# Performance work log

Hardware: AMD Instinct MI355X
Metric: run time of the kernel (lower is better)

The kernel has to match this reference:

```python
import jax, jax.numpy as jnp
import numpy as np

B, SEQ, PRED, ENC = 32, 720, 96, 321
LAYERS, SCALE = 2, 2
SEG = [48, 24]
D = [512, 256]
SNX = [SEQ // s for s in SEG]   # [15, 30]
SNY = [PRED // s for s in SEG]  # [2, 4]


def _gru(x, h, Wih, Whh, bih, bhh):
    # torch.nn.GRUCell math
    gi = x @ Wih.T + bih
    gh = h @ Whh.T + bhh
    i_r, i_z, i_n = jnp.split(gi, 3, axis=-1)
    h_r, h_z, h_n = jnp.split(gh, 3, axis=-1)
    r = jax.nn.sigmoid(i_r + h_r)
    z = jax.nn.sigmoid(i_z + h_z)
    n = jnp.tanh(i_n + r * h_n)
    return (1.0 - z) * n + z * h


def setup_inputs():
    key = jax.random.key(0)
    ks = iter(jax.random.split(key, 40))
    inp = {"x": jax.random.normal(next(ks), (B, SEQ, ENC), jnp.float32)}
    sc = 0.02
    for i in range(LAYERS):
        d, s = D[i], SEG[i]
        inp[f"W_emb{i}"] = jax.random.normal(next(ks), (d, s), jnp.float32) * sc
        inp[f"b_emb{i}"] = jnp.zeros((d,), jnp.float32)
        inp[f"Wih{i}"] = jax.random.normal(next(ks), (3 * d, d), jnp.float32) * sc
        inp[f"Whh{i}"] = jax.random.normal(next(ks), (3 * d, d), jnp.float32) * sc
        inp[f"bih{i}"] = jnp.zeros((3 * d,), jnp.float32)
        inp[f"bhh{i}"] = jnp.zeros((3 * d,), jnp.float32)
        inp[f"Wpred{i}"] = jax.random.normal(next(ks), (s, d), jnp.float32) * sc
        inp[f"bpred{i}"] = jnp.zeros((s,), jnp.float32)
        inp[f"pos{i}"] = jax.random.normal(next(ks), (SNY[i], d // 2), jnp.float32)
        inp[f"chan{i}"] = jax.random.normal(next(ks), (ENC, d // 2), jnp.float32)
    return inp


def _forward(x, params):
    seq_last = jax.lax.stop_gradient(x[:, -1:, :])   # [B,1,ENC] (detached in torch)
    xc = (x - seq_last).transpose(0, 2, 1)            # [B,ENC,SEQ]
    out = jnp.zeros((B, PRED, ENC), x.dtype)
    for i in range(LAYERS):
        p = params[i]
        d, s, T, S = D[i], SEG[i], SNX[i], SNY[i]
        # value embedding: [B*ENC, T, seg_len] -> [B*ENC, T, d]
        xe = jax.nn.relu(jnp.einsum('nts,ds->ntd', xc.reshape(-1, T, s), p['W_emb']) + p['b_emb'])
        if i == 0:
            seq = xe.transpose(1, 0, 2)   # all seg_num_x[0] segments in order
        else:
            # faithful to source: finer layer always consumes segments 0..scale^(i+1)-1
            # once per outer step, seg_num_x[0] times in total
            k = SCALE ** (i + 1)
            idx = np.tile(np.arange(k), SNX[0])
            seq = xe[:, idx].transpose(1, 0, 2)
        h0 = jnp.zeros((xe.shape[0], d), x.dtype)
        step = lambda h, xt: (_gru(xt, h, p['Wih'], p['Whh'], p['bih'], p['bhh']), None)
        h_fin, _ = jax.lax.scan(step, h0, seq)   # [B*ENC, d]
        # decoder: seg_num_y independent GRU cell applications (no carried state)
        half = d // 2
        pos = jnp.concatenate([
            jnp.broadcast_to(p['pos'][None], (ENC, S, half)),
            jnp.broadcast_to(p['chan'][:, None], (ENC, S, half))], axis=-1).reshape(ENC * S, d)
        pos = jnp.tile(pos, (B, 1)).reshape(S, B * ENC, d)   # contiguous chunks per step
        hn = jnp.repeat(h_fin, S, axis=0).reshape(S, B * ENC, d)
        hy = _gru(pos, hn, p['Wih'], p['Whh'], p['bih'], p['bhh'])   # [S, B*ENC, d]
        y = hy.reshape(S * B * ENC, d) @ p['Wpred'].T + p['bpred']   # [S*B*ENC, seg_len]
        y = y.reshape(-1, ENC, PRED).transpose(0, 2, 1)              # [B, PRED, ENC]
        out = out + y + seq_last
    return out / LAYERS


def reference(x, W_emb0, b_emb0, Wih0, Whh0, bih0, bhh0, Wpred0, bpred0, pos0, chan0,
              W_emb1, b_emb1, Wih1, Whh1, bih1, bhh1, Wpred1, bpred1, pos1, chan1):
    params = [
        dict(W_emb=W_emb0, b_emb=b_emb0, Wih=Wih0, Whh=Whh0, bih=bih0, bhh=bhh0,
             Wpred=Wpred0, bpred=bpred0, pos=pos0, chan=chan0),
        dict(W_emb=W_emb1, b_emb=b_emb1, Wih=Wih1, Whh=Whh1, bih=bih1, bhh=bhh1,
             Wpred=Wpred1, bpred=bpred1, pos=pos1, chan=chan1),
    ]
    return _forward(x, params)
```

## Files before the change

### kernel.cpp

```cpp
#include <hip/hip_runtime.h>
#include <math.h>


#define NB     10272
#define MP     10368
#define ENC_   321
#define SEQ_   720
#define PRED_  96
#define BATCH_ 32

typedef long long i64;
typedef unsigned short u16;
typedef unsigned int u32;
using bf16x8 = __attribute__((ext_vector_type(8))) short;
using f32x4  = __attribute__((ext_vector_type(4))) float;

#define AS1 __attribute__((address_space(1)))
#define AS3 __attribute__((address_space(3)))
#define GLOAD16(g, l) __builtin_amdgcn_global_load_lds((const AS1 void*)(g), (AS3 void*)(l), 16, 0, 0)

__device__ __forceinline__ float bf2f(u16 u) {
    union { u32 i; float f; } v; v.i = ((u32)u) << 16; return v.f;
}
__device__ __forceinline__ u16 f2bf(float f) {
    union { float f; u32 i; } v; v.f = f;
    return (u16)((v.i + 0x7fff + ((v.i >> 16) & 1)) >> 16);
}
__device__ __forceinline__ float sigf(float x) {
    x = fminf(fmaxf(x, -30.f), 30.f);
    return 1.f / (1.f + __expf(-x));
}
__device__ __forceinline__ float tanhfast(float x) {
    x = fminf(fmaxf(x, -15.f), 15.f);
    float e = __expf(2.f * x);
    return (e - 1.f) / (e + 1.f);
}
__device__ __forceinline__ void swz(int idx, int NXT, int NYT, int& mt, int& nt) {
    int per = NYT * 8;
    int grp = idx / per;
    int base = grp * 8;
    int mg = NXT - base; if (mg > 8) mg = 8;
    int rem = idx - grp * per;
    mt = base + rem % mg;
    nt = rem / mg;
}

__global__ __launch_bounds__(256) void zero2_kernel(float* __restrict__ a,
                                                    u16* __restrict__ b, i64 n) {
    i64 i = (i64)blockIdx.x * 256 + threadIdx.x;
    if (i < n) { a[i] = 0.f; b[i] = 0; }
}

__global__ __launch_bounds__(256) void convert_pad(const float* __restrict__ src,
                                                   u16* __restrict__ dst,
                                                   int R, int C, int Rp, int Cp) {
    i64 idx = (i64)blockIdx.x * 256 + threadIdx.x;
    i64 total = (i64)Rp * Cp;
    if (idx >= total) return;
    int r = (int)(idx / Cp);
    int c = (int)(idx - (i64)r * Cp);
    dst[idx] = (r < R && c < C) ? f2bf(src[(i64)r * C + c]) : (u16)0;
}

__global__ __launch_bounds__(256) void seg_gather_bf(const float* __restrict__ x,
                                                     u16* __restrict__ dst,
                                                     int t0, int T, int s, int Kp) {
    i64 idx = (i64)blockIdx.x * 256 + threadIdx.x;
    i64 per_t = (i64)MP * Kp;
    i64 total = (i64)T * per_t;
    if (idx >= total) return;
    int t = (int)(idx / per_t);
    i64 rem = idx - (i64)t * per_t;
    int j = (int)(rem / MP);
    int n = (int)(rem - (i64)j * MP);
    float v = 0.f;
    if (n < NB && j < s) {
        int b = n / ENC_, e = n - b * ENC_;
        const float* xb = x + (i64)b * SEQ_ * ENC_ + e;
        v = xb[(i64)((t0 + t) * s + j) * ENC_] - xb[(i64)(SEQ_ - 1) * ENC_];
    }
    dst[((i64)t * MP + n) * Kp + j] = f2bf(v);
}

__global__ __launch_bounds__(256) void pmat_fill_bf(const float* __restrict__ pos,
                                                    const float* __restrict__ chan,
                                                    u16* __restrict__ dst,
                                                    int S, int d, int Rp) {
    i64 idx = (i64)blockIdx.x * 256 + threadIdx.x;
    i64 total = (i64)Rp * d;
    if (idx >= total) return;
    int row = (int)(idx / d);
    int c = (int)(idx - (i64)row * d);
    float v = 0.f;
    if (row < ENC_ * S) {
        int e = row / S, sy = row - e * S;
        int half = d >> 1;
        v = (c < half) ? pos[sy * half + c] : chan[e * half + (c - half)];
    }
    dst[idx] = f2bf(v);
}

__global__ __launch_bounds__(256) void out_kernel(const float* __restrict__ x,
                                                  const float* __restrict__ y0,
                                                  const float* __restrict__ y1,
                                                  float* __restrict__ out) {
    int idx = blockIdx.x * 256 + threadIdx.x;
    const int total = BATCH_ * PRED_ * ENC_;
    if (idx >= total) return;
    int b = idx / (PRED_ * ENC_);
    int r = idx - b * (PRED_ * ENC_);
    int p = r / ENC_;
    int e = r - p * ENC_;
    int n = b * ENC_ + e;
    float sl = x[(i64)b * SEQ_ * ENC_ + (i64)(SEQ_ - 1) * ENC_ + e];
    out[idx] = sl + 0.5f * (y0[(i64)n * PRED_ + p] + y1[(i64)n * PRED_ + p]);
}

template<int MODE>
__global__ __launch_bounds__(256) void gemm_bf16mfma(const u16* __restrict__ A,
                                                     const u16* __restrict__ B,
                                                     const float* __restrict__ bias,
                                                     void* __restrict__ Cp,
                                                     int K, int Mstore, int Nstore,
                                                     int ldc, int NXT, int NYT) {
    __shared__ u16 smA[128 * 64];
    __shared__ u16 smB[128 * 64];
    const int tid = threadIdx.x;
    const int w = tid >> 6, l = tid & 63;
    int mt, nt; swz(blockIdx.x, NXT, NYT, mt, nt);
    const int m0 = mt * 128, n0 = nt * 128;
    const int srow = (l >> 3) & 7, pch = l & 7;
    const int cch = pch ^ srow;
    const u16* ga[4]; const u16* gb[4];
#pragma unroll
    for (int r = 0; r < 4; ++r) {
        int seg = r * 4 + w;
        ga[r] = A + (i64)(m0 + seg * 8 + srow) * K + cch * 8;
        gb[r] = B + (i64)(n0 + seg * 8 + srow) * K + cch * 8;
    }
    f32x4 acc[4][4] = {};
    const int lr = l & 15, lg = l >> 4;
    const int wm = (w >> 1) * 64, wn = (w & 1) * 64;
    for (int kk = 0; kk < K; kk += 64) {
#pragma unroll
        for (int r = 0; r < 4; ++r) { GLOAD16(ga[r], smA + (r * 4 + w) * 512); ga[r] += 64; }
#pragma unroll
        for (int r = 0; r < 4; ++r) { GLOAD16(gb[r], smB + (r * 4 + w) * 512); gb[r] += 64; }
        __syncthreads();
#pragma unroll
        for (int s = 0; s < 2; ++s) {
            const int ph = ((s * 4 + lg) ^ (lr & 7)) * 8;
            bf16x8 av[4], bv[4];
#pragma unroll
            for (int i = 0; i < 4; ++i)
                av[i] = *(const bf16x8*)(smA + (wm + i * 16 + lr) * 64 + ph);
#pragma unroll
            for (int j = 0; j < 4; ++j)
                bv[j] = *(const bf16x8*)(smB + (wn + j * 16 + lr) * 64 + ph);
#pragma unroll
            for (int i = 0; i < 4; ++i)
#pragma unroll
                for (int j = 0; j < 4; ++j)
                    acc[i][j] = __builtin_amdgcn_mfma_f32_16x16x32_bf16(av[i], bv[j], acc[i][j], 0, 0, 0);
        }
        __syncthreads();
    }
#pragma unroll
    for (int i = 0; i < 4; ++i) {
        int mbase = m0 + wm + i * 16 + 4 * lg;
#pragma unroll
        for (int j = 0; j < 4; ++j) {
            int c = n0 + wn + j * 16 + lr;
            if (c >= Nstore) continue;
            float bs = bias[c];
#pragma unroll
            for (int r = 0; r < 4; ++r) {
                int mm = mbase + r;
                if (mm < Mstore) {
                    float v = acc[i][j][r] + bs;
                    if (MODE == 2) v = fmaxf(v, 0.f);
                    if (MODE == 0) ((float*)Cp)[(i64)mm * ldc + c] = v;
                    else           ((u16*)Cp)[(i64)mm * ldc + c] = f2bf(v);
                }
            }
        }
    }
}

template<int D>
__global__ __launch_bounds__(256, 3) void gru_step(const u16* __restrict__ xe,
                                                   const u16* __restrict__ hsrc,
                                                   const u16* __restrict__ Wih,
                                                   const u16* __restrict__ Whh,
                                                   const float* __restrict__ bih,
                                                   const float* __restrict__ bhh,
                                                   f32x4* __restrict__ hfrag,
                                                   u16* __restrict__ hdst) {
    constexpr int NCT = D / 16;
    __shared__ u16 smA[64 * 64];
    __shared__ u16 smB[3 * 64 * 64];
    const int tid = threadIdx.x;
    const int w = tid >> 6, l = tid & 63;
    const int m0 = blockIdx.x * 64;
    const int c0 = blockIdx.y * 64;
    const int srow = (l >> 3) & 7, pch = l & 7;
    const int cch = pch ^ srow;
    const int lr = l & 15, lg = l >> 4;
    f32x4 aR[4] = {}, aZ[4] = {}, aNI[4] = {}, aNH[4] = {};
#pragma unroll
    for (int phase = 0; phase < 2; ++phase) {
        const u16* Abase = phase ? hsrc : xe;
        const u16* Bbase = phase ? Whh : Wih;
        const u16* ga[2]; const u16* gb[6];
#pragma unroll
        for (int r = 0; r < 2; ++r)
            ga[r] = Abase + (i64)(m0 + (r * 4 + w) * 8 + srow) * D + cch * 8;
#pragma unroll
        for (int q = 0; q < 6; ++q) {
            int gs = q * 4 + w;
            int g = gs >> 3, sp = gs & 7;
            gb[q] = Bbase + (i64)(g * D + c0 + sp * 8 + srow) * D + cch * 8;
        }
        for (int kk = 0; kk < D; kk += 64) {
#pragma unroll
            for (int r = 0; r < 2; ++r) { GLOAD16(ga[r], smA + (r * 4 + w) * 512); ga[r] += 64; }
#pragma unroll
            for (int q = 0; q < 6; ++q) { GLOAD16(gb[q], smB + (q * 4 + w) * 512); gb[q] += 64; }
            __syncthreads();
#pragma unroll
            for (int s = 0; s < 2; ++s) {
                const int phs = ((s * 4 + lg) ^ (lr & 7)) * 8;
                bf16x8 av = *(const bf16x8*)(smA + (w * 16 + lr) * 64 + phs);
#pragma unroll
                for (int j = 0; j < 4; ++j) {
                    bf16x8 b0 = *(const bf16x8*)(smB + 0 * 4096 + (j * 16 + lr) * 64 + phs);
                    bf16x8 b1 = *(const bf16x8*)(smB + 1 * 4096 + (j * 16 + lr) * 64 + phs);
                    bf16x8 b2 = *(const bf16x8*)(smB + 2 * 4096 + (j * 16 + lr) * 64 + phs);
                    aR[j] = __builtin_amdgcn_mfma_f32_16x16x32_bf16(av, b0, aR[j], 0, 0, 0);
                    aZ[j] = __builtin_amdgcn_mfma_f32_16x16x32_bf16(av, b1, aZ[j], 0, 0, 0);
                    if (phase == 0)
                        aNI[j] = __builtin_amdgcn_mfma_f32_16x16x32_bf16(av, b2, aNI[j], 0, 0, 0);
                    else
                        aNH[j] = __builtin_amdgcn_mfma_f32_16x16x32_bf16(av, b2, aNH[j], 0, 0, 0);
                }
            }
            __syncthreads();
        }
    }
    const int Trow = (m0 >> 4) + w;
    const int rowb = m0 + w * 16 + 4 * lg;
#pragma unroll
    for (int j = 0; j < 4; ++j) {
        const int cc = c0 + j * 16 + lr;
        const i64 tb = (i64)Trow * NCT + ((c0 >> 4) + j);
        f32x4 ho = hfrag[tb * 64 + l];
        float bR = bih[cc] + bhh[cc];
        float bZ = bih[D + cc] + bhh[D + cc];
        float bNI = bih[2 * D + cc];
        float bNH = bhh[2 * D + cc];
        f32x4 hn;
#pragma unroll
        for (int r = 0; r < 4; ++r) {
            float rr = sigf(aR[j][r] + bR);
            float zz = sigf(aZ[j][r] + bZ);
            float nn = tanhfast(aNI[j][r] + bNI + rr * (aNH[j][r] + bNH));
            hn[r] = (1.f - zz) * nn + zz * ho[r];
        }
        hfrag[tb * 64 + l] = hn;
#pragma unroll
        for (int r = 0; r < 4; ++r)
            hdst[(i64)(rowb + r) * D + cc] = f2bf(hn[r]);
    }
}

template<int D>
__global__ __launch_bounds__(256, 3) void gru_step_h(const u16* __restrict__ gi,
                                                     const u16* __restrict__ hsrc,
                                                     const u16* __restrict__ Whh,
                                                     const float* __restrict__ bhh,
                                                     f32x4* __restrict__ hfrag,
                                                     u16* __restrict__ hdst) {
    constexpr int NCT = D / 16;
    __shared__ u16 smA[64 * 64];
    __shared__ u16 smB[3 * 64 * 64];
    const int tid = threadIdx.x;
    const int w = tid >> 6, l = tid & 63;
    const int m0 = blockIdx.x * 64;
    const int c0 = blockIdx.y * 64;
    const int srow = (l >> 3) & 7, pch = l & 7;
    const int cch = pch ^ srow;
    const int lr = l & 15, lg = l >> 4;
    f32x4 aR[4] = {}, aZ[4] = {}, aNH[4] = {};
    const u16* ga[2]; const u16* gb[6];
#pragma unroll
    for (int r = 0; r < 2; ++r)
        ga[r] = hsrc + (i64)(m0 + (r * 4 + w) * 8 + srow) * D + cch * 8;
#pragma unroll
    for (int q = 0; q < 6; ++q) {
        int gs = q * 4 + w;
        int g = gs >> 3, sp = gs & 7;
        gb[q] = Whh + (i64)(g * D + c0 + sp * 8 + srow) * D + cch * 8;
    }
    for (int kk = 0; kk < D; kk += 64) {
#pragma unroll
        for (int r = 0; r < 2; ++r) { GLOAD16(ga[r], smA + (r * 4 + w) * 512); ga[r] += 64; }
#pragma unroll
        for (int q = 0; q < 6; ++q) { GLOAD16(gb[q], smB + (q * 4 + w) * 512); gb[q] += 64; }
        __syncthreads();
#pragma unroll
        for (int s = 0; s < 2; ++s) {
            const int phs = ((s * 4 + lg) ^ (lr & 7)) * 8;
            bf16x8 av = *(const bf16x8*)(smA + (w * 16 + lr) * 64 + phs);
#pragma unroll
            for (int j = 0; j < 4; ++j) {
                bf16x8 b0 = *(const bf16x8*)(smB + 0 * 4096 + (j * 16 + lr) * 64 + phs);
                bf16x8 b1 = *(const bf16x8*)(smB + 1 * 4096 + (j * 16 + lr) * 64 + phs);
                bf16x8 b2 = *(const bf16x8*)(smB + 2 * 4096 + (j * 16 + lr) * 64 + phs);
                aR[j] = __builtin_amdgcn_mfma_f32_16x16x32_bf16(av, b0, aR[j], 0, 0, 0);
                aZ[j] = __builtin_amdgcn_mfma_f32_16x16x32_bf16(av, b1, aZ[j], 0, 0, 0);
                aNH[j] = __builtin_amdgcn_mfma_f32_16x16x32_bf16(av, b2, aNH[j], 0, 0, 0);
            }
        }
        __syncthreads();
    }
    const int Trow = (m0 >> 4) + w;
    const int rowb = m0 + w * 16 + 4 * lg;
#pragma unroll
    for (int j = 0; j < 4; ++j) {
        const int cc = c0 + j * 16 + lr;
        const i64 tb = (i64)Trow * NCT + ((c0 >> 4) + j);
        f32x4 ho = hfrag[tb * 64 + l];
        float bR = bhh[cc];
        float bZ = bhh[D + cc];
        float bNH = bhh[2 * D + cc];
        f32x4 hn;
#pragma unroll
        for (int r = 0; r < 4; ++r) {
            const u16* gp = gi + (i64)(rowb + r) * 3 * D + cc;
            float rr = sigf(bf2f(gp[0]) + aR[j][r] + bR);
            float zz = sigf(bf2f(gp[D]) + aZ[j][r] + bZ);
            float nn = tanhfast(bf2f(gp[2 * D]) + rr * (aNH[j][r] + bNH));
            hn[r] = (1.f - zz) * nn + zz * ho[r];
        }
        hfrag[tb * 64 + l] = hn;
#pragma unroll
        for (int r = 0; r < 4; ++r)
            hdst[(i64)(rowb + r) * D + cc] = f2bf(hn[r]);
    }
}

template<int D, int S>
__global__ __launch_bounds__(256) void gru_dec(const u16* __restrict__ Asrc,
                                               const u16* __restrict__ Whh,
                                               const float* __restrict__ bhh,
                                               const u16* __restrict__ gi,
                                               const f32x4* __restrict__ hfrag,
                                               u16* __restrict__ hy) {
    constexpr int NCT = D / 16;
    constexpr int NYT = D / 64;
    __shared__ u16 smA[128 * 64];
    __shared__ u16 smB[3 * 64 * 64];
    const int tid = threadIdx.x;
    const int w = tid >> 6, l = tid & 63;
    int mt, nt; swz(blockIdx.x, 81, NYT, mt, nt);
    const int m0 = mt * 128;
    const int c0 = nt * 64;
    const int srow = (l >> 3) & 7, pch = l & 7;
    const int cch = pch ^ srow;
    const u16* ga[4]; const u16* gb[6];
#pragma unroll
    for (int r = 0; r < 4; ++r)
        ga[r] = Asrc + (i64)(m0 + (r * 4 + w) * 8 + srow) * D + cch * 8;
#pragma unroll
    for (int q = 0; q < 6; ++q) {
        int gs = q * 4 + w;
        int g = gs >> 3, sp = gs & 7;
        gb[q] = Whh + (i64)(g * D + c0 + sp * 8 + srow) * D + cch * 8;
    }
    f32x4 acc[3][4][2] = {};
    const int lr = l & 15, lg = l >> 4;
    const int wm = (w >> 1) * 64, wc = (w & 1) * 32;
    for (int kk = 0; kk < D; kk += 64) {
#pragma unroll
        for (int r = 0; r < 4; ++r) { GLOAD16(ga[r], smA + (r * 4 + w) * 512); ga[r] += 64; }
#pragma unroll
        for (int q = 0; q < 6; ++q) { GLOAD16(gb[q], smB + (q * 4 + w) * 512); gb[q] += 64; }
        __syncthreads();
#pragma unroll
        for (int s = 0; s < 2; ++s) {
            const int ph = ((s * 4 + lg) ^ (lr & 7)) * 8;
            bf16x8 av[4], bv[3][2];
#pragma unroll
            for (int i = 0; i < 4; ++i)
                av[i] = *(const bf16x8*)(smA + (wm + i * 16 + lr) * 64 + ph);
#pragma unroll
            for (int g = 0; g < 3; ++g)
#pragma unroll
                for (int j = 0; j < 2; ++j)
                    bv[g][j] = *(const bf16x8*)(smB + g * 4096 + (wc + j * 16 + lr) * 64 + ph);
#pragma unroll
            for (int g = 0; g < 3; ++g)
#pragma unroll
                for (int i = 0; i < 4; ++i)
#pragma unroll
                    for (int j = 0; j < 2; ++j)
                        acc[g][i][j] = __builtin_amdgcn_mfma_f32_16x16x32_bf16(av[i], bv[g][j], acc[g][i][j], 0, 0, 0);
        }
        __syncthreads();
    }
#pragma unroll
    for (int i = 0; i < 4; ++i) {
        const int Trow = (m0 + wm + 16 * i) >> 4;
        const int rowb = m0 + wm + 16 * i + 4 * lg;
#pragma unroll
        for (int j = 0; j < 2; ++j) {
            const int cc = c0 + wc + 16 * j + lr;
            const int ct = (c0 + wc + 16 * j) >> 4;
            const i64 tb = (i64)Trow * NCT + ct;
            float b0 = bhh[cc], b1 = bhh[D + cc], b2 = bhh[2 * D + cc];
            f32x4 ho = hfrag[tb * 64 + l];
#pragma unroll
            for (int r = 0; r < 4; ++r) {
                int mm = rowb + r;
                if (mm >= NB) continue;
                int e = mm % ENC_;
                float hr = acc[0][i][j][r] + b0;
                float hz = acc[1][i][j][r] + b1;
                float hn2 = acc[2][i][j][r] + b2;
#pragma unroll
                for (int sy = 0; sy < S; ++sy) {
                    i64 gib = (i64)(e * S + sy) * 3 * D + cc;
                    float rr = sigf(bf2f(gi[gib]) + hr);
                    float zz = sigf(bf2f(gi[gib + D]) + hz);
                    float nn = tanhfast(bf2f(gi[gib + 2 * D]) + rr * hn2);
                    hy[((i64)mm * S + sy) * D + cc] = f2bf((1.f - zz) * nn + zz * ho[r]);
                }
            }
        }
    }
}

extern "C" void kernel_launch(void* const* d_in, const int* in_sizes, int n_in,
                              void* d_out, int out_size, void* d_ws, size_t ws_size,
                              hipStream_t stream) {
    const float* x      = (const float*)d_in[0];
    const float* W_emb0 = (const float*)d_in[1];
    const float* b_emb0 = (const float*)d_in[2];
    const float* Wih0   = (const float*)d_in[3];
    const float* Whh0   = (const float*)d_in[4];
    const float* bih0   = (const float*)d_in[5];
    const float* bhh0   = (const float*)d_in[6];
    const float* Wpred0 = (const float*)d_in[7];
    const float* bpred0 = (const float*)d_in[8];
    const float* pos0   = (const float*)d_in[9];
    const float* chan0  = (const float*)d_in[10];
    const float* W_emb1 = (const float*)d_in[11];
    const float* b_emb1 = (const float*)d_in[12];
    const float* Wih1   = (const float*)d_in[13];
    const float* Whh1   = (const float*)d_in[14];
    const float* bih1   = (const float*)d_in[15];
    const float* bhh1   = (const float*)d_in[16];
    const float* Wpred1 = (const float*)d_in[17];
    const float* bpred1 = (const float*)d_in[18];
    const float* pos1   = (const float*)d_in[19];
    const float* chan1  = (const float*)d_in[20];
    float* out = (float*)d_out;

    i64 off = 0;
    char* base = (char*)d_ws;
    auto alloc = [&](i64 bytes) -> void* {
        void* p = base + off; off += (bytes + 255) & ~(i64)255; return p;
    };
    float* f_hfrag = (float*)alloc((i64)MP * 512 * 4);
    u16*   f_mirA  = (u16*)  alloc((i64)MP * 512 * 2);
    u16*   f_mirB  = (u16*)  alloc((i64)MP * 512 * 2);
    u16*   wih0b   = (u16*)  alloc((i64)1536 * 512 * 2);
    u16*   whh0b   = (u16*)  alloc((i64)1536 * 512 * 2);
    u16*   wih1b   = (u16*)  alloc((i64)768 * 256 * 2);
    u16*   whh1b   = (u16*)  alloc((i64)768 * 256 * 2);
    u16*   we0b    = (u16*)  alloc((i64)512 * 64 * 2);
    u16*   we1b    = (u16*)  alloc((i64)256 * 64 * 2);
    u16*   wp0b    = (u16*)  alloc((i64)128 * 512 * 2);
    u16*   wp1b    = (u16*)  alloc((i64)128 * 256 * 2);
    u16*   f_pm0   = (u16*)  alloc((i64)768 * 512 * 2);
    u16*   f_pm1   = (u16*)  alloc((i64)1408 * 256 * 2);
    u16*   f_gidec = (u16*)  alloc((i64)768 * 1536 * 2);
    u16*   f_hy    = (u16*)  alloc((i64)4 * NB * 256 * 2);
    float* f_y0    = (float*)alloc((i64)NB * 96 * 4);
    float* f_y1    = (float*)alloc((i64)NB * 96 * 4);
    i64 fixed = off;

    char* R = base + fixed;
    i64 a1 = (((i64)4 * MP * 64 * 2) + 255) & ~(i64)255;
    i64 a2 = (((i64)4 * MP * 256 * 2) + 255) & ~(i64)255;
    i64 a3 = (i64)4 * MP * 768 * 2;
    i64 R1 = a1 + a2 + a3;
    u16* f_seg1 = (u16*)R;
    u16* f_xe1  = (u16*)(R + a1);
    u16* f_gi1  = (u16*)(R + a1 + a2);
    int gsz = 1;
    {
        const int cand[4] = {15, 5, 3, 2};
        for (int ii = 0; ii < 4; ++ii) {
            i64 need = (i64)cand[ii] * MP * (64 + 512) * 2 + 2 * 256;
            i64 tot = fixed + (need > R1 ? need : R1);
            if (tot <= (i64)ws_size) { gsz = cand[ii]; break; }
        }
    }
    u16* f_seg0 = (u16*)R;
    i64 s1 = (((i64)gsz * MP * 64 * 2) + 255) & ~(i64)255;
    u16* f_xe0 = (u16*)(R + s1);

    auto cvt = [&](const float* s, u16* dst, int Rr, int C, int Rp, int Cp) {
        i64 tot = (i64)Rp * Cp;
        convert_pad<<<(int)((tot + 255) / 256), 256, 0, stream>>>(s, dst, Rr, C, Rp, Cp);
    };
    auto gemmN = [&](const u16* A, const u16* B, const float* bias, void* C,
                     int gx, int Nc, int K, int Mstore, int ldc, int mode) {
        int NYT = (Nc + 127) / 128;
        dim3 g(gx * NYT);
        if (mode == 0)      gemm_bf16mfma<0><<<g, 256, 0, stream>>>(A, B, bias, C, K, Mstore, Nc, ldc, gx, NYT);
        else if (mode == 1) gemm_bf16mfma<1><<<g, 256, 0, stream>>>(A, B, bias, C, K, Mstore, Nc, ldc, gx, NYT);
        else                gemm_bf16mfma<2><<<g, 256, 0, stream>>>(A, B, bias, C, K, Mstore, Nc, ldc, gx, NYT);
    };

    cvt(Wih0, wih0b, 1536, 512, 1536, 512);
    cvt(Whh0, whh0b, 1536, 512, 1536, 512);
    cvt(Wih1, wih1b, 768, 256, 768, 256);
    cvt(Whh1, whh1b, 768, 256, 768, 256);
    cvt(W_emb0, we0b, 512, 48, 512, 64);
    cvt(W_emb1, we1b, 256, 24, 256, 64);
    cvt(Wpred0, wp0b, 48, 512, 128, 512);
    cvt(Wpred1, wp1b, 24, 256, 128, 256);
    pmat_fill_bf<<<(int)(((i64)768 * 512 + 255) / 256), 256, 0, stream>>>(pos0, chan0, f_pm0, 2, 512, 768);
    pmat_fill_bf<<<(int)(((i64)1408 * 256 + 255) / 256), 256, 0, stream>>>(pos1, chan1, f_pm1, 4, 256, 1408);

    {
        i64 n = (i64)MP * 512;
        zero2_kernel<<<(int)((n + 255) / 256), 256, 0, stream>>>(f_hfrag, f_mirA, n);
    }
    for (int t0 = 0; t0 < 15;) {
        int g = 15 - t0 < gsz ? 15 - t0 : gsz;
        i64 tot = (i64)g * MP * 64;
        seg_gather_bf<<<(int)((tot + 255) / 256), 256, 0, stream>>>(x, f_seg0, t0, g, 48, 64);
        gemmN(f_seg0, we0b, b_emb0, f_xe0, g * 81, 512, 64, g * MP, 512, 2);
        for (int s = 0; s < g; ++s) {
            int tg = t0 + s;
            const u16* Asrc = (tg & 1) ? f_mirB : f_mirA;
            u16* Adst = (tg & 1) ? f_mirA : f_mirB;
            gru_step<512><<<dim3(162, 8), 256, 0, stream>>>(
                f_xe0 + (i64)s * MP * 512, Asrc, wih0b, whh0b, bih0, bhh0,
                (f32x4*)f_hfrag, Adst);
        }
        t0 += g;
    }
    gemmN(f_pm0, wih0b, bih0, f_gidec, 6, 1536, 512, 642, 1536, 1);
    gru_dec<512, 2><<<dim3(81 * 8), 256, 0, stream>>>(
        f_mirB, whh0b, bhh0, f_gidec, (const f32x4*)f_hfrag, f_hy);
    gemmN(f_hy, wp0b, bpred0, f_y0, 161, 48, 512, 2 * NB, 48, 0);

    {
        i64 n = (i64)MP * 256;
        zero2_kernel<<<(int)((n + 255) / 256), 256, 0, stream>>>(f_hfrag, f_mirA, n);
    }
    {
        i64 tot = (i64)4 * MP * 64;
        seg_gather_bf<<<(int)((tot + 255) / 256), 256, 0, stream>>>(x, f_seg1, 0, 4, 24, 64);
    }
    gemmN(f_seg1, we1b, b_emb1, f_xe1, 324, 256, 64, 4 * MP, 256, 2);
    gemmN(f_xe1, wih1b, bih1, f_gi1, 324, 768, 256, 4 * MP, 768, 1);
    for (int t = 0; t < 60; ++t) {
        const u16* Asrc = (t & 1) ? f_mirB : f_mirA;
        u16* Adst = (t & 1) ? f_mirA : f_mirB;
        gru_step_h<256><<<dim3(162, 4), 256, 0, stream>>>(
            f_gi1 + (i64)(t & 3) * MP * 768, Asrc, whh1b, bhh1,
            (f32x4*)f_hfrag, Adst);
    }
    gemmN(f_pm1, wih1b, bih1, f_gidec, 11, 768, 256, 1284, 768, 1);
    gru_dec<256, 4><<<dim3(81 * 4), 256, 0, stream>>>(
        f_mirA, whh1b, bhh1, f_gidec, (const f32x4*)f_hfrag, f_hy);
    gemmN(f_hy, wp1b, bpred1, f_y1, 321, 24, 256, 4 * NB, 24, 0);

    out_kernel<<<(BATCH_ * PRED_ * ENC_ + 255) / 256, 256, 0, stream>>>(x, f_y0, f_y1, out);
}
```

Baseline: 2.373 ms.

## Fuse layer-1 GRU recurrence into a persistent scan kernel with LDS-resident state

Replaces 60 per-step gru_step_h launches with one gru_scan kernel. Each block owns 64 rows across all 256 columns, keeps the hidden state in registers and a double-buffered LDS copy, and streams Whh tiles through a triple-buffered global_load_lds pipeline. This removes per-step launch overhead, the global round-trip of the hidden state, and the separate zeroing kernel. The cost is only 162 blocks (less parallelism than 162x4), and Whh is re-streamed by every block at every step.

New measurement: 3.997 ms. 1.68x slower.

```diff
diff --git a/kernel.cpp b/kernel.cpp
--- a/kernel.cpp
+++ b/kernel.cpp
@@ -18,6 +18,7 @@
 #define AS1 __attribute__((address_space(1)))
 #define AS3 __attribute__((address_space(3)))
 #define GLOAD16(g, l) __builtin_amdgcn_global_load_lds((const AS1 void*)(g), (AS3 void*)(l), 16, 0, 0)
+#define MFMA16(a, b, c) __builtin_amdgcn_mfma_f32_16x16x32_bf16(a, b, c, 0, 0, 0)
 
 __device__ __forceinline__ float bf2f(u16 u) {
     union { u32 i; float f; } v; v.i = ((u32)u) << 16; return v.f;
@@ -161,7 +162,7 @@
             for (int i = 0; i < 4; ++i)
 #pragma unroll
                 for (int j = 0; j < 4; ++j)
-                    acc[i][j] = __builtin_amdgcn_mfma_f32_16x16x32_bf16(av[i], bv[j], acc[i][j], 0, 0, 0);
+                    acc[i][j] = MFMA16(av[i], bv[j], acc[i][j]);
         }
         __syncthreads();
     }
@@ -236,12 +237,12 @@
                     bf16x8 b0 = *(const bf16x8*)(smB + 0 * 4096 + (j * 16 + lr) * 64 + phs);
                     bf16x8 b1 = *(const bf16x8*)(smB + 1 * 4096 + (j * 16 + lr) * 64 + phs);
                     bf16x8 b2 = *(const bf16x8*)(smB + 2 * 4096 + (j * 16 + lr) * 64 + phs);
-                    aR[j] = __builtin_amdgcn_mfma_f32_16x16x32_bf16(av, b0, aR[j], 0, 0, 0);
-                    aZ[j] = __builtin_amdgcn_mfma_f32_16x16x32_bf16(av, b1, aZ[j], 0, 0, 0);
+                    aR[j] = MFMA16(av, b0, aR[j]);
+                    aZ[j] = MFMA16(av, b1, aZ[j]);
                     if (phase == 0)
-                        aNI[j] = __builtin_amdgcn_mfma_f32_16x16x32_bf16(av, b2, aNI[j], 0, 0, 0);
+                        aNI[j] = MFMA16(av, b2, aNI[j]);
                     else
-                        aNH[j] = __builtin_amdgcn_mfma_f32_16x16x32_bf16(av, b2, aNH[j], 0, 0, 0);
+                        aNH[j] = MFMA16(av, b2, aNH[j]);
                 }
             }
             __syncthreads();
@@ -273,79 +274,116 @@
     }
 }
 
-template<int D>
-__global__ __launch_bounds__(256, 3) void gru_step_h(const u16* __restrict__ gi,
-                                                     const u16* __restrict__ hsrc,
-                                                     const u16* __restrict__ Whh,
-                                                     const float* __restrict__ bhh,
-                                                     f32x4* __restrict__ hfrag,
-                                                     u16* __restrict__ hdst) {
+template<int D, int T>
+__global__ __launch_bounds__(256) void gru_scan(const u16* __restrict__ gi,
+                                                const u16* __restrict__ Whh,
+                                                const float* __restrict__ bhh,
+                                                f32x4* __restrict__ hfrag,
+                                                u16* __restrict__ hdst) {
     constexpr int NCT = D / 16;
-    __shared__ u16 smA[64 * 64];
-    __shared__ u16 smB[3 * 64 * 64];
+    __shared__ u16 hb[2][4][64 * 64];
+    __shared__ u16 sB[3][192 * 64];
     const int tid = threadIdx.x;
     const int w = tid >> 6, l = tid & 63;
     const int m0 = blockIdx.x * 64;
-    const int c0 = blockIdx.y * 64;
     const int srow = (l >> 3) & 7, pch = l & 7;
     const int cch = pch ^ srow;
     const int lr = l & 15, lg = l >> 4;
-    f32x4 aR[4] = {}, aZ[4] = {}, aNH[4] = {};
-    const u16* ga[2]; const u16* gb[6];
-#pragma unroll
-    for (int r = 0; r < 2; ++r)
-        ga[r] = hsrc + (i64)(m0 + (r * 4 + w) * 8 + srow) * D + cch * 8;
+    const int rowl = w * 16 + 4 * lg;
+
+    const u16* gq[6];
 #pragma unroll
     for (int q = 0; q < 6; ++q) {
         int gs = q * 4 + w;
-        int g = gs >> 3, sp = gs & 7;
-        gb[q] = Whh + (i64)(g * D + c0 + sp * 8 + srow) * D + cch * 8;
-    }
-    for (int kk = 0; kk < D; kk += 64) {
-#pragma unroll
-        for (int r = 0; r < 2; ++r) { GLOAD16(ga[r], smA + (r * 4 + w) * 512); ga[r] += 64; }
-#pragma unroll
-        for (int q = 0; q < 6; ++q) { GLOAD16(gb[q], smB + (q * 4 + w) * 512); gb[q] += 64; }
-        __syncthreads();
-#pragma unroll
-        for (int s = 0; s < 2; ++s) {
-            const int phs = ((s * 4 + lg) ^ (lr & 7)) * 8;
-            bf16x8 av = *(const bf16x8*)(smA + (w * 16 + lr) * 64 + phs);
+        int gate = gs >> 3, sp = gs & 7;
+        gq[q] = Whh + (i64)(gate * D + sp * 8 + srow) * D + cch * 8;
+    }
+    f32x4 hm[4][4];
+#pragma unroll
+    for (int a = 0; a < 4; ++a)
+#pragma unroll
+        for (int b = 0; b < 4; ++b) hm[a][b] = f32x4{0.f, 0.f, 0.f, 0.f};
+    {
+        u32* p = (u32*)&hb[0][0][0];
+        for (int i = tid; i < 8192; i += 256) p[i] = 0;
+    }
+    auto STAGE = [&](int g) {
+        int s16 = g & 15;
+        i64 off = (i64)((s16 >> 2) * 64) * D + (i64)(s16 & 3) * 64;
+        u16* dst = &sB[g % 3][0];
+#pragma unroll
+        for (int q = 0; q < 6; ++q)
+            GLOAD16(gq[q] + off, dst + (q * 4 + w) * 512);
+    };
+    STAGE(0); STAGE(1);
+
+    for (int t = 0; t < T; ++t) {
+        const int hcur = t & 1, hnxt = hcur ^ 1;
+        const u16* gis = gi + (i64)(t & 3) * MP * 3 * D;
+#pragma unroll
+        for (int c0i = 0; c0i < 4; ++c0i) {
+            f32x4 aR[4] = {}, aZ[4] = {}, aNH[4] = {};
+#pragma unroll
+            for (int kk = 0; kk < 4; ++kk) {
+                asm volatile("s_waitcnt vmcnt(6) lgkmcnt(0)" ::: "memory");
+                __builtin_amdgcn_s_barrier();
+                __builtin_amdgcn_sched_barrier(0);
+                const int g = t * 16 + c0i * 4 + kk;
+                STAGE(g + 2);
+                const u16* bp = &sB[g % 3][0];
+                const u16* ap = &hb[hcur][kk][0];
+#pragma unroll
+                for (int s = 0; s < 2; ++s) {
+                    const int phs = ((s * 4 + lg) ^ (lr & 7)) * 8;
+                    bf16x8 av = *(const bf16x8*)(ap + (w * 16 + lr) * 64 + phs);
+#pragma unroll
+                    for (int j = 0; j < 4; ++j) {
+                        bf16x8 b0 = *(const bf16x8*)(bp + (0 * 64 + j * 16 + lr) * 64 + phs);
+                        bf16x8 b1 = *(const bf16x8*)(bp + (1 * 64 + j * 16 + lr) * 64 + phs);
+                        bf16x8 b2 = *(const bf16x8*)(bp + (2 * 64 + j * 16 + lr) * 64 + phs);
+                        aR[j] = MFMA16(av, b0, aR[j]);
+                        aZ[j] = MFMA16(av, b1, aZ[j]);
+                        aNH[j] = MFMA16(av, b2, aNH[j]);
+                    }
+                }
+            }
 #pragma unroll
             for (int j = 0; j < 4; ++j) {
-                bf16x8 b0 = *(const bf16x8*)(smB + 0 * 4096 + (j * 16 + lr) * 64 + phs);
-                bf16x8 b1 = *(const bf16x8*)(smB + 1 * 4096 + (j * 16 + lr) * 64 + phs);
-                bf16x8 b2 = *(const bf16x8*)(smB + 2 * 4096 + (j * 16 + lr) * 64 + phs);
-                aR[j] = __builtin_amdgcn_mfma_f32_16x16x32_bf16(av, b0, aR[j], 0, 0, 0);
-                aZ[j] = __builtin_amdgcn_mfma_f32_16x16x32_bf16(av, b1, aZ[j], 0, 0, 0);
-                aNH[j] = __builtin_amdgcn_mfma_f32_16x16x32_bf16(av, b2, aNH[j], 0, 0, 0);
+                const int cc = c0i * 64 + j * 16 + lr;
+                const float bR = bhh[cc];
+                const float bZ = bhh[D + cc];
+                const float bN = bhh[2 * D + cc];
+#pragma unroll
+                for (int r = 0; r < 4; ++r) {
+                    const u16* gp = gis + (i64)(m0 + rowl + r) * 3 * D + cc;
+                    float rr = sigf(bf2f(gp[0]) + aR[j][r] + bR);
+                    float zz = sigf(bf2f(gp[D]) + aZ[j][r] + bZ);
+                    float nn = tanhfast(bf2f(gp[2 * D]) + rr * (aNH[j][r] + bN));
+                    hm[c0i][j][r] = (1.f - zz) * nn + zz * hm[c0i][j][r];
+                }
+                const int cl = j * 16 + lr;
+#pragma unroll
+                for (int r = 0; r < 4; ++r) {
+                    const int row = rowl + r;
+                    hb[hnxt][c0i][row * 64 + (((cl >> 3) ^ (row & 7)) << 3) + (cl & 7)]
+                        = f2bf(hm[c0i][j][r]);
+                }
             }
         }
-        __syncthreads();
-    }
-    const int Trow = (m0 >> 4) + w;
-    const int rowb = m0 + w * 16 + 4 * lg;
-#pragma unroll
-    for (int j = 0; j < 4; ++j) {
-        const int cc = c0 + j * 16 + lr;
-        const i64 tb = (i64)Trow * NCT + ((c0 >> 4) + j);
-        f32x4 ho = hfrag[tb * 64 + l];
-        float bR = bhh[cc];
-        float bZ = bhh[D + cc];
-        float bNH = bhh[2 * D + cc];
-        f32x4 hn;
-#pragma unroll
-        for (int r = 0; r < 4; ++r) {
-            const u16* gp = gi + (i64)(rowb + r) * 3 * D + cc;
-            float rr = sigf(bf2f(gp[0]) + aR[j][r] + bR);
-            float zz = sigf(bf2f(gp[D]) + aZ[j][r] + bZ);
-            float nn = tanhfast(bf2f(gp[2 * D]) + rr * (aNH[j][r] + bNH));
-            hn[r] = (1.f - zz) * nn + zz * ho[r];
-        }
-        hfrag[tb * 64 + l] = hn;
-#pragma unroll
-        for (int r = 0; r < 4; ++r)
-            hdst[(i64)(rowb + r) * D + cc] = f2bf(hn[r]);
+        if (t == T - 1) {
+            const int Trow = (m0 >> 4) + w;
+#pragma unroll
+            for (int c0i = 0; c0i < 4; ++c0i)
+#pragma unroll
+                for (int j = 0; j < 4; ++j) {
+                    const i64 tb = (i64)Trow * NCT + (c0i * 4 + j);
+                    hfrag[tb * 64 + l] = hm[c0i][j];
+                    const int cc = c0i * 64 + j * 16 + lr;
+#pragma unroll
+                    for (int r = 0; r < 4; ++r)
+                        hdst[(i64)(m0 + rowl + r) * D + cc] = f2bf(hm[c0i][j][r]);
+                }
+        }
     }
 }
 
@@ -404,7 +442,7 @@
                 for (int i = 0; i < 4; ++i)
 #pragma unroll
                     for (int j = 0; j < 2; ++j)
-                        acc[g][i][j] = __builtin_amdgcn_mfma_f32_16x16x32_bf16(av[i], bv[g][j], acc[g][i][j], 0, 0, 0);
+                        acc[g][i][j] = MFMA16(av[i], bv[g][j], acc[g][i][j]);
         }
         __syncthreads();
     }
@@ -560,22 +598,13 @@
     gemmN(f_hy, wp0b, bpred0, f_y0, 161, 48, 512, 2 * NB, 48, 0);
 
     {
-        i64 n = (i64)MP * 256;
-        zero2_kernel<<<(int)((n + 255) / 256), 256, 0, stream>>>(f_hfrag, f_mirA, n);
-    }
-    {
         i64 tot = (i64)4 * MP * 64;
         seg_gather_bf<<<(int)((tot + 255) / 256), 256, 0, stream>>>(x, f_seg1, 0, 4, 24, 64);
     }
     gemmN(f_seg1, we1b, b_emb1, f_xe1, 324, 256, 64, 4 * MP, 256, 2);
     gemmN(f_xe1, wih1b, bih1, f_gi1, 324, 768, 256, 4 * MP, 768, 1);
-    for (int t = 0; t < 60; ++t) {
-        const u16* Asrc = (t & 1) ? f_mirB : f_mirA;
-        u16* Adst = (t & 1) ? f_mirA : f_mirB;
-        gru_step_h<256><<<dim3(162, 4), 256, 0, stream>>>(
-            f_gi1 + (i64)(t & 3) * MP * 768, Asrc, whh1b, bhh1,
-            (f32x4*)f_hfrag, Adst);
-    }
+    gru_scan<256, 60><<<dim3(162), 256, 0, stream>>>(
+        f_gi1, whh1b, bhh1, (f32x4*)f_hfrag, f_mirA);
     gemmN(f_pm1, wih1b, bih1, f_gidec, 11, 768, 256, 1284, 768, 1);
     gru_dec<256, 4><<<dim3(81 * 4), 256, 0, stream>>>(
         f_mirA, whh1b, bhh1, f_gidec, (const f32x4*)f_hfrag, f_hy);
```

## Read previous hidden state from LDS and skip fp32 state writes until last step

Applied to the files above, without the earlier changes.

The GRU step kernels now take the previous hidden state from the bf16 h tile already streamed into shared memory (an extra LDS copy at the matching k-tile) instead of reading the fp32 fragment buffer. The fp32 fragment state is only written on the final timestep of each layer. The layer-1 input-gate GEMM also gains an epilogue that stores in MFMA fragment order, so the step kernel can load gate inputs with vector loads. This cuts global traffic per recurrent step, but the blend term now uses bf16-rounded h, which lowers precision, and the extra smH buffer adds LDS use that may reduce occupancy.

Measured after the change: 2.223 ms. -6.3%, faster.

```diff
diff --git a/kernel.cpp b/kernel.cpp
--- a/kernel.cpp
+++ b/kernel.cpp
@@ -14,10 +14,12 @@
 typedef unsigned int u32;
 using bf16x8 = __attribute__((ext_vector_type(8))) short;
 using f32x4  = __attribute__((ext_vector_type(4))) float;
+using u16x4  = __attribute__((ext_vector_type(4))) unsigned short;
 
 #define AS1 __attribute__((address_space(1)))
 #define AS3 __attribute__((address_space(3)))
 #define GLOAD16(g, l) __builtin_amdgcn_global_load_lds((const AS1 void*)(g), (AS3 void*)(l), 16, 0, 0)
+#define MFMA16(a, b, c) __builtin_amdgcn_mfma_f32_16x16x32_bf16(a, b, c, 0, 0, 0)
 
 __device__ __forceinline__ float bf2f(u16 u) {
     union { u32 i; float f; } v; v.i = ((u32)u) << 16; return v.f;
@@ -161,9 +163,27 @@
             for (int i = 0; i < 4; ++i)
 #pragma unroll
                 for (int j = 0; j < 4; ++j)
-                    acc[i][j] = __builtin_amdgcn_mfma_f32_16x16x32_bf16(av[i], bv[j], acc[i][j], 0, 0, 0);
+                    acc[i][j] = MFMA16(av[i], bv[j], acc[i][j]);
         }
         __syncthreads();
+    }
+    if (MODE == 3) {
+        const int NCTG = ldc >> 4;
+#pragma unroll
+        for (int i = 0; i < 4; ++i) {
+            int mt16 = (m0 + wm + i * 16) >> 4;
+#pragma unroll
+            for (int j = 0; j < 4; ++j) {
+                int cb = n0 + wn + j * 16;
+                if (cb >= Nstore) continue;
+                float bs = bias[cb + lr];
+                u16x4 sv;
+#pragma unroll
+                for (int r = 0; r < 4; ++r) sv[r] = f2bf(acc[i][j][r] + bs);
+                *(u16x4*)((u16*)Cp + ((i64)mt16 * NCTG + (cb >> 4)) * 256 + l * 4) = sv;
+            }
+        }
+        return;
     }
 #pragma unroll
     for (int i = 0; i < 4; ++i) {
@@ -195,10 +215,12 @@
                                                    const float* __restrict__ bih,
                                                    const float* __restrict__ bhh,
                                                    f32x4* __restrict__ hfrag,
-                                                   u16* __restrict__ hdst) {
+                                                   u16* __restrict__ hdst,
+                                                   int writeFrag) {
     constexpr int NCT = D / 16;
     __shared__ u16 smA[64 * 64];
     __shared__ u16 smB[3 * 64 * 64];
+    __shared__ u16 smH[64 * 64];
     const int tid = threadIdx.x;
     const int w = tid >> 6, l = tid & 63;
     const int m0 = blockIdx.x * 64;
@@ -223,7 +245,13 @@
         }
         for (int kk = 0; kk < D; kk += 64) {
 #pragma unroll
-            for (int r = 0; r < 2; ++r) { GLOAD16(ga[r], smA + (r * 4 + w) * 512); ga[r] += 64; }
+            for (int r = 0; r < 2; ++r) GLOAD16(ga[r], smA + (r * 4 + w) * 512);
+            if (phase == 1 && kk == c0) {
+#pragma unroll
+                for (int r = 0; r < 2; ++r) GLOAD16(ga[r], smH + (r * 4 + w) * 512);
+            }
+#pragma unroll
+            for (int r = 0; r < 2; ++r) ga[r] += 64;
 #pragma unroll
             for (int q = 0; q < 6; ++q) { GLOAD16(gb[q], smB + (q * 4 + w) * 512); gb[q] += 64; }
             __syncthreads();
@@ -236,12 +264,12 @@
                     bf16x8 b0 = *(const bf16x8*)(smB + 0 * 4096 + (j * 16 + lr) * 64 + phs);
                     bf16x8 b1 = *(const bf16x8*)(smB + 1 * 4096 + (j * 16 + lr) * 64 + phs);
                     bf16x8 b2 = *(const bf16x8*)(smB + 2 * 4096 + (j * 16 + lr) * 64 + phs);
-                    aR[j] = __builtin_amdgcn_mfma_f32_16x16x32_bf16(av, b0, aR[j], 0, 0, 0);
-                    aZ[j] = __builtin_amdgcn_mfma_f32_16x16x32_bf16(av, b1, aZ[j], 0, 0, 0);
+                    aR[j] = MFMA16(av, b0, aR[j]);
+                    aZ[j] = MFMA16(av, b1, aZ[j]);
                     if (phase == 0)
-                        aNI[j] = __builtin_amdgcn_mfma_f32_16x16x32_bf16(av, b2, aNI[j], 0, 0, 0);
+                        aNI[j] = MFMA16(av, b2, aNI[j]);
                     else
-                        aNH[j] = __builtin_amdgcn_mfma_f32_16x16x32_bf16(av, b2, aNH[j], 0, 0, 0);
+                        aNH[j] = MFMA16(av, b2, aNH[j]);
                 }
             }
             __syncthreads();
@@ -253,7 +281,6 @@
     for (int j = 0; j < 4; ++j) {
         const int cc = c0 + j * 16 + lr;
         const i64 tb = (i64)Trow * NCT + ((c0 >> 4) + j);
-        f32x4 ho = hfrag[tb * 64 + l];
         float bR = bih[cc] + bhh[cc];
         float bZ = bih[D + cc] + bhh[D + cc];
         float bNI = bih[2 * D + cc];
@@ -261,12 +288,15 @@
         f32x4 hn;
 #pragma unroll
         for (int r = 0; r < 4; ++r) {
+            const int lrow = w * 16 + 4 * lg + r;
+            const int lcol = j * 16 + lr;
+            float ho = bf2f(smH[lrow * 64 + ((((lcol >> 3)) ^ (lrow & 7)) << 3) + (lcol & 7)]);
             float rr = sigf(aR[j][r] + bR);
             float zz = sigf(aZ[j][r] + bZ);
             float nn = tanhfast(aNI[j][r] + bNI + rr * (aNH[j][r] + bNH));
-            hn[r] = (1.f - zz) * nn + zz * ho[r];
-        }
-        hfrag[tb * 64 + l] = hn;
+            hn[r] = (1.f - zz) * nn + zz * ho;
+        }
+        if (writeFrag) hfrag[tb * 64 + l] = hn;
 #pragma unroll
         for (int r = 0; r < 4; ++r)
             hdst[(i64)(rowb + r) * D + cc] = f2bf(hn[r]);
@@ -279,10 +309,13 @@
                                                      const u16* __restrict__ Whh,
                                                      const float* __restrict__ bhh,
                                                      f32x4* __restrict__ hfrag,
-                                                     u16* __restrict__ hdst) {
+                                                     u16* __restrict__ hdst,
+                                                     int writeFrag) {
     constexpr int NCT = D / 16;
+    constexpr int NCTG = 3 * D / 16;
     __shared__ u16 smA[64 * 64];
     __shared__ u16 smB[3 * 64 * 64];
+    __shared__ u16 smH[64 * 64];
     const int tid = threadIdx.x;
     const int w = tid >> 6, l = tid & 63;
     const int m0 = blockIdx.x * 64;
@@ -303,7 +336,13 @@
     }
     for (int kk = 0; kk < D; kk += 64) {
 #pragma unroll
-        for (int r = 0; r < 2; ++r) { GLOAD16(ga[r], smA + (r * 4 + w) * 512); ga[r] += 64; }
+        for (int r = 0; r < 2; ++r) GLOAD16(ga[r], smA + (r * 4 + w) * 512);
+        if (kk == c0) {
+#pragma unroll
+            for (int r = 0; r < 2; ++r) GLOAD16(ga[r], smH + (r * 4 + w) * 512);
+        }
+#pragma unroll
+        for (int r = 0; r < 2; ++r) ga[r] += 64;
 #pragma unroll
         for (int q = 0; q < 6; ++q) { GLOAD16(gb[q], smB + (q * 4 + w) * 512); gb[q] += 64; }
         __syncthreads();
@@ -316,33 +355,39 @@
                 bf16x8 b0 = *(const bf16x8*)(smB + 0 * 4096 + (j * 16 + lr) * 64 + phs);
                 bf16x8 b1 = *(const bf16x8*)(smB + 1 * 4096 + (j * 16 + lr) * 64 + phs);
                 bf16x8 b2 = *(const bf16x8*)(smB + 2 * 4096 + (j * 16 + lr) * 64 + phs);
-                aR[j] = __builtin_amdgcn_mfma_f32_16x16x32_bf16(av, b0, aR[j], 0, 0, 0);
-                aZ[j] = __builtin_amdgcn_mfma_f32_16x16x32_bf16(av, b1, aZ[j], 0, 0, 0);
-                aNH[j] = __builtin_amdgcn_mfma_f32_16x16x32_bf16(av, b2, aNH[j], 0, 0, 0);
+                aR[j] = MFMA16(av, b0, aR[j]);
+                aZ[j] = MFMA16(av, b1, aZ[j]);
+                aNH[j] = MFMA16(av, b2, aNH[j]);
             }
         }
         __syncthreads();
     }
     const int Trow = (m0 >> 4) + w;
     const int rowb = m0 + w * 16 + 4 * lg;
+    const i64 gbase = (i64)Trow * NCTG * 256 + l * 4;
 #pragma unroll
     for (int j = 0; j < 4; ++j) {
         const int cc = c0 + j * 16 + lr;
-        const i64 tb = (i64)Trow * NCT + ((c0 >> 4) + j);
-        f32x4 ho = hfrag[tb * 64 + l];
+        const int ct = (c0 >> 4) + j;
+        const i64 tb = (i64)Trow * NCT + ct;
+        u16x4 g0 = *(const u16x4*)(gi + gbase + (i64)(0 * NCT + ct) * 256);
+        u16x4 g1 = *(const u16x4*)(gi + gbase + (i64)(1 * NCT + ct) * 256);
+        u16x4 g2 = *(const u16x4*)(gi + gbase + (i64)(2 * NCT + ct) * 256);
         float bR = bhh[cc];
         float bZ = bhh[D + cc];
         float bNH = bhh[2 * D + cc];
         f32x4 hn;
 #pragma unroll
         for (int r = 0; r < 4; ++r) {
-            const u16* gp = gi + (i64)(rowb + r) * 3 * D + cc;
-            float rr = sigf(bf2f(gp[0]) + aR[j][r] + bR);
-            float zz = sigf(bf2f(gp[D]) + aZ[j][r] + bZ);
-            float nn = tanhfast(bf2f(gp[2 * D]) + rr * (aNH[j][r] + bNH));
-            hn[r] = (1.f - zz) * nn + zz * ho[r];
-        }
-        hfrag[tb * 64 + l] = hn;
+            const int lrow = w * 16 + 4 * lg + r;
+            const int lcol = j * 16 + lr;
+            float ho = bf2f(smH[lrow * 64 + ((((lcol >> 3)) ^ (lrow & 7)) << 3) + (lcol & 7)]);
+            float rr = sigf(bf2f(g0[r]) + aR[j][r] + bR);
+            float zz = sigf(bf2f(g1[r]) + aZ[j][r] + bZ);
+            float nn = tanhfast(bf2f(g2[r]) + rr * (aNH[j][r] + bNH));
+            hn[r] = (1.f - zz) * nn + zz * ho;
+        }
+        if (writeFrag) hfrag[tb * 64 + l] = hn;
 #pragma unroll
         for (int r = 0; r < 4; ++r)
             hdst[(i64)(rowb + r) * D + cc] = f2bf(hn[r]);
@@ -404,7 +449,7 @@
                 for (int i = 0; i < 4; ++i)
 #pragma unroll
                     for (int j = 0; j < 2; ++j)
-                        acc[g][i][j] = __builtin_amdgcn_mfma_f32_16x16x32_bf16(av[i], bv[g][j], acc[g][i][j], 0, 0, 0);
+                        acc[g][i][j] = MFMA16(av[i], bv[g][j], acc[g][i][j]);
         }
         __syncthreads();
     }
@@ -521,7 +566,8 @@
         dim3 g(gx * NYT);
         if (mode == 0)      gemm_bf16mfma<0><<<g, 256, 0, stream>>>(A, B, bias, C, K, Mstore, Nc, ldc, gx, NYT);
         else if (mode == 1) gemm_bf16mfma<1><<<g, 256, 0, stream>>>(A, B, bias, C, K, Mstore, Nc, ldc, gx, NYT);
-        else                gemm_bf16mfma<2><<<g, 256, 0, stream>>>(A, B, bias, C, K, Mstore, Nc, ldc, gx, NYT);
+        else if (mode == 2) gemm_bf16mfma<2><<<g, 256, 0, stream>>>(A, B, bias, C, K, Mstore, Nc, ldc, gx, NYT);
+        else                gemm_bf16mfma<3><<<g, 256, 0, stream>>>(A, B, bias, C, K, Mstore, Nc, ldc, gx, NYT);
     };
 
     cvt(Wih0, wih0b, 1536, 512, 1536, 512);
@@ -550,7 +596,7 @@
             u16* Adst = (tg & 1) ? f_mirA : f_mirB;
             gru_step<512><<<dim3(162, 8), 256, 0, stream>>>(
                 f_xe0 + (i64)s * MP * 512, Asrc, wih0b, whh0b, bih0, bhh0,
-                (f32x4*)f_hfrag, Adst);
+                (f32x4*)f_hfrag, Adst, (tg == 14) ? 1 : 0);
         }
         t0 += g;
     }
@@ -568,13 +614,13 @@
         seg_gather_bf<<<(int)((tot + 255) / 256), 256, 0, stream>>>(x, f_seg1, 0, 4, 24, 64);
     }
     gemmN(f_seg1, we1b, b_emb1, f_xe1, 324, 256, 64, 4 * MP, 256, 2);
-    gemmN(f_xe1, wih1b, bih1, f_gi1, 324, 768, 256, 4 * MP, 768, 1);
+    gemmN(f_xe1, wih1b, bih1, f_gi1, 324, 768, 256, 4 * MP, 768, 3);
     for (int t = 0; t < 60; ++t) {
         const u16* Asrc = (t & 1) ? f_mirB : f_mirA;
         u16* Adst = (t & 1) ? f_mirA : f_mirB;
         gru_step_h<256><<<dim3(162, 4), 256, 0, stream>>>(
             f_gi1 + (i64)(t & 3) * MP * 768, Asrc, whh1b, bhh1,
-            (f32x4*)f_hfrag, Adst);
+            (f32x4*)f_hfrag, Adst, (t == 59) ? 1 : 0);
     }
     gemmN(f_pm1, wih1b, bih1, f_gidec, 11, 768, 256, 1284, 768, 1);
     gru_dec<256, 4><<<dim3(81 * 4), 256, 0, stream>>>(
```
